# Performance work log

Hardware: AMD Instinct MI355X
Metric: run time of the kernel (lower is better)

## Reference

```python
import jax, jax.numpy as jnp
import numpy as np
from jax import lax

DIM = 128
HEADS = 4
B, H, W = 8, 128, 128


def conv1x1(x, w, b):
    # x: [B,C,H,W], w: [O,I,1,1]
    y = lax.conv_general_dilated(x, w, (1, 1), 'VALID',
                                 dimension_numbers=('NCHW', 'OIHW', 'NCHW'))
    return y + b[None, :, None, None]


def dwconv3x3(x, w, b):
    # depthwise: w: [C,1,3,3], groups=C
    C = x.shape[1]
    y = lax.conv_general_dilated(x, w, (1, 1), ((1, 1), (1, 1)),
                                 dimension_numbers=('NCHW', 'OIHW', 'NCHW'),
                                 feature_group_count=C)
    return y + b[None, :, None, None]


def setup_inputs() -> dict:
    key = jax.random.key(0)
    ks = jax.random.split(key, 7)
    s = 0.02
    return {
        'x': jax.random.normal(ks[0], (B, DIM, H, W), jnp.float32),
        'qkv_w': jax.random.normal(ks[1], (3 * DIM, DIM, 1, 1), jnp.float32) * s,
        'qkv_b': jnp.zeros((3 * DIM,), jnp.float32),
        'dw_w': jax.random.normal(ks[2], (3 * DIM, 1, 3, 3), jnp.float32) * s,
        'dw_b': jnp.zeros((3 * DIM,), jnp.float32),
        'proj_w': jax.random.normal(ks[3], (DIM, DIM, 1, 1), jnp.float32) * s,
        'proj_b': jnp.zeros((DIM,), jnp.float32),
        'temperature': jnp.ones((HEADS, 1, 1, 1), jnp.float32),
    }


def reference(x, qkv_w, qkv_b, dw_w, dw_b, proj_w, proj_b, temperature):
    b, C, h, w = x.shape
    heads = temperature.shape[0]
    c = C // heads

    qkv = dwconv3x3(conv1x1(x, qkv_w, qkv_b), dw_w, dw_b)
    q, k, v = jnp.split(qkv, 3, axis=1)

    # b (head c) h w -> b head c h w
    q = q.reshape(b, heads, c, h, w)
    k = k.reshape(b, heads, c, h, w)
    v = v.reshape(b, heads, c, h, w)

    # L2-normalize along H (axis=-2), matching torch F.normalize eps=1e-12
    eps = 1e-12
    q = q / jnp.maximum(jnp.linalg.norm(q, axis=-2, keepdims=True), eps)
    k = k / jnp.maximum(jnp.linalg.norm(k, axis=-2, keepdims=True), eps)

    # attn[b,n,c,j,k] = sum_i q[b,n,c,i,j] * k_[b,n,c,i,k]  -> [b,head,c,W,W]
    attn = jnp.einsum('bncij,bncik->bncjk', q, k) * temperature
    attn = jax.nn.softmax(attn, axis=-2)

    # out[b,n,c,i,k] = sum_j v[b,n,c,i,j] * attn[b,n,c,j,k]
    out = jnp.einsum('bncij,bncjk->bncik', v, attn)
    out = out.reshape(b, C, h, w)
    return conv1x1(out, proj_w, proj_b)
```

## Files before the change

### kernel.cpp

```cpp
#include <hip/hip_runtime.h>

typedef unsigned short u16;
typedef unsigned int   u32;

typedef short bf16x8 __attribute__((ext_vector_type(8)));
typedef float f32x4  __attribute__((ext_vector_type(4)));

__device__ __forceinline__ float bf2f(u16 u) { return __uint_as_float(((u32)u) << 16); }
__device__ __forceinline__ u16 f2bf(float f) {
    u32 u = __float_as_uint(f);
    return (u16)((u + 0x7fffu + ((u >> 16) & 1u)) >> 16);
}

#define MFMA16(a, b, c) __builtin_amdgcn_mfma_f32_16x16x32_bf16(a, b, c, 0, 0, 0)

__global__ __launch_bounds__(256, 4) void k_xpose(const float* __restrict__ x,
                                                  u16* __restrict__ xT) {
    __shared__ u16 Xs[128 * 128];
    const int ptile = blockIdx.x, b = blockIdx.y;
    const int t = threadIdx.x;
    const float* xb = x + (((size_t)b) << 21) + ptile * 128;
#pragma unroll
    for (int i = 0; i < 16; ++i) {
        int idx = i * 256 + t;
        int ci = idx >> 5, pq = idx & 31;
        float4 v = *(const float4*)(xb + (((size_t)ci) << 14) + pq * 4);
        u32 lo = (u32)f2bf(v.x) | ((u32)f2bf(v.y) << 16);
        u32 hi = (u32)f2bf(v.z) | ((u32)f2bf(v.w) << 16);
        uint2 pk; pk.x = lo; pk.y = hi;
        int cq = ci >> 3;
        *(uint2*)(&Xs[ci * 128 + ((pq ^ cq) << 2)]) = pk;
    }
    __syncthreads();
    u16* ob = xT + (((size_t)b) << 21) + ((size_t)(ptile * 128)) * 128;
#pragma unroll
    for (int j = 0; j < 8; ++j) {
        int p = j * 16 + (t >> 4), cq = t & 15;
        u16 tmp[8];
#pragma unroll
        for (int c = 0; c < 8; ++c) {
            int ci = cq * 8 + c;
            tmp[c] = Xs[ci * 128 + (((p >> 2) ^ cq) << 2) + (p & 3)];
        }
        *(uint4*)(&ob[(size_t)p * 128 + cq * 8]) = *(const uint4*)tmp;
    }
}

template <bool CM>
__global__ __launch_bounds__(512, 6) void k_qkv_t(const u16* __restrict__ xT,
                                                  const float* __restrict__ w,
                                                  const float* __restrict__ bias,
                                                  u16* __restrict__ out1,
                                                  int cgbase) {
    extern __shared__ char smem[];
    u16* Bt = (u16*)smem;
    u16* Cs = Bt + 2048 * 8;
    const int h = blockIdx.x, cg = blockIdx.y + cgbase, b = blockIdx.z;
    const int t = threadIdx.x;

    const u16* xb = xT + (((size_t)b) << 21) + (CM ? (h << 7) : (h << 14));
#pragma unroll
    for (int i = 0; i < 4; ++i) {
        int slot = i * 512 + t;
        int p = slot >> 4, g = slot & 15;
        int gg = g ^ (p & 15);
        uint4 v = *(const uint4*)(&xb[(CM ? (p << 14) : (p << 7)) + gg * 8]);
        *(uint4*)(&Bt[slot * 8]) = v;
    }

    const int wave = t >> 6, lane = t & 63, m16 = lane & 15, quad = lane >> 4;
    bf16x8 afr[4];
    {
        const float* wp0 = w + (size_t)(cg * 128 + wave * 16 + m16) * 128 + quad * 8;
#pragma unroll
        for (int kk = 0; kk < 4; ++kk) {
            float4 w0 = *(const float4*)(wp0 + kk * 32);
            float4 w1 = *(const float4*)(wp0 + kk * 32 + 4);
            bf16x8 a;
            a[0] = (short)f2bf(w0.x); a[1] = (short)f2bf(w0.y);
            a[2] = (short)f2bf(w0.z); a[3] = (short)f2bf(w0.w);
            a[4] = (short)f2bf(w1.x); a[5] = (short)f2bf(w1.y);
            a[6] = (short)f2bf(w1.z); a[7] = (short)f2bf(w1.w);
            afr[kk] = a;
        }
    }
    __syncthreads();

    f32x4 acc[8] = {};
#pragma unroll
    for (int kk = 0; kk < 4; ++kk) {
        const int g = kk * 4 + quad;
#pragma unroll
        for (int nt = 0; nt < 8; ++nt) {
            int p = nt * 16 + m16;
            bf16x8 bf = *(const bf16x8*)(&Bt[p * 128 + ((g ^ (p & 15)) << 3)]);
            acc[nt] = MFMA16(afr[kk], bf, acc[nt]);
        }
    }

    float bv[4];
#pragma unroll
    for (int r = 0; r < 4; ++r) bv[r] = bias[cg * 128 + wave * 16 + quad * 4 + r];

    u16* ob = out1 + (((size_t)(b * 384 + cg * 128)) << 14) + (h << 7);

    if (wave < 4) {
#pragma unroll
        for (int nt = 0; nt < 8; ++nt) {
            int p = nt * 16 + m16;
#pragma unroll
            for (int r = 0; r < 4; ++r)
                Cs[(wave * 16 + quad * 4 + r) * 136 + p] = f2bf(acc[nt][r] + bv[r]);
        }
    }
    __syncthreads();
#pragma unroll
    for (int it = 0; it < 2; ++it) {
        int idx = it * 512 + t;
        int co = idx >> 4, cp = idx & 15;
        *(uint4*)(&ob[((size_t)co << 14) + cp * 8]) = *(const uint4*)(&Cs[co * 136 + cp * 8]);
    }
    __syncthreads();

    if (wave >= 4) {
#pragma unroll
        for (int nt = 0; nt < 8; ++nt) {
            int p = nt * 16 + m16;
#pragma unroll
            for (int r = 0; r < 4; ++r)
                Cs[((wave - 4) * 16 + quad * 4 + r) * 136 + p] = f2bf(acc[nt][r] + bv[r]);
        }
    }
    __syncthreads();
    u16* ob2 = ob + ((size_t)64 << 14);
#pragma unroll
    for (int it = 0; it < 2; ++it) {
        int idx = it * 512 + t;
        int co = idx >> 4, cp = idx & 15;
        *(uint4*)(&ob2[((size_t)co << 14) + cp * 8]) = *(const uint4*)(&Cs[co * 136 + cp * 8]);
    }
}

__global__ __launch_bounds__(512, 4) void k_attn(const u16* __restrict__ qkv,
                                                 const float* __restrict__ dww,
                                                 const float* __restrict__ dwb,
                                                 const float* __restrict__ temp,
                                                 u16* __restrict__ outp) {
    extern __shared__ char smem[];
    u16* R0 = (u16*)smem;
    u16* Qt = (u16*)(smem + 36864);
    float* rqk = (float*)(smem + 69632);
    u16* Pt = Qt;
    u16* Osh = R0;

    const int ch = blockIdx.x, b = blockIdx.y;
    const int head = ch >> 5;
    const int t = threadIdx.x;
    const size_t qoff = ((size_t)(b * 384 + ch)) << 14;
    const size_t koff = qoff + ((size_t)128 << 14);
    const size_t voff = qoff + ((size_t)256 << 14);

    const int wave = t >> 6, lane = t & 63, m16 = lane & 15, quad = lane >> 4;
    const int wr = wave * 16 + m16;

#pragma unroll
    for (int i = 0; i < 4; ++i) {
        int idx = i * 512 + t;
        int r = idx >> 4, c16 = idx & 15;
        *(uint4*)(&R0[r * 144 + 8 + c16 * 8]) =
            *(const uint4*)(&qkv[voff + ((size_t)r << 7) + c16 * 8]);
    }
    if (t < 256) {
        int r = t >> 1, side = t & 1;
        uint4 z = {0, 0, 0, 0};
        *(uint4*)(&R0[r * 144 + side * 136]) = z;
    }
    __syncthreads();

    bf16x8 vfr[4];
    {
        float w9[9];
        const float* wp = dww + (size_t)(256 + ch) * 9;
#pragma unroll
        for (int i = 0; i < 9; ++i) w9[i] = wp[i];
        const float gb = dwb[256 + ch];
#pragma unroll
        for (int kk = 0; kk < 4; ++kk) {
            const int c0 = quad * 8 + kk * 32;
            float acc[8];
#pragma unroll
            for (int c = 0; c < 8; ++c) acc[c] = gb;
#pragma unroll
            for (int dy = 0; dy < 3; ++dy) {
                int rr = wr + dy - 1;
                if ((unsigned)rr < 128u) {
                    const u16* row = &R0[rr * 144 + 8 + c0];
                    float v0 = bf2f(row[-1]);
                    uint4 m = *(const uint4*)row;
                    float v1 = bf2f((u16)(m.x & 0xffff)), v2 = bf2f((u16)(m.x >> 16));
                    float v3 = bf2f((u16)(m.y & 0xffff)), v4 = bf2f((u16)(m.y >> 16));
                    float v5 = bf2f((u16)(m.z & 0xffff)), v6 = bf2f((u16)(m.z >> 16));
                    float v7 = bf2f((u16)(m.w & 0xffff)), v8 = bf2f((u16)(m.w >> 16));
                    float v9 = bf2f(row[8]);
                    const float w0 = w9[dy * 3], w1 = w9[dy * 3 + 1], w2 = w9[dy * 3 + 2];
                    acc[0] += w0 * v0 + w1 * v1 + w2 * v2;
                    acc[1] += w0 * v1 + w1 * v2 + w2 * v3;
                    acc[2] += w0 * v2 + w1 * v3 + w2 * v4;
                    acc[3] += w0 * v3 + w1 * v4 + w2 * v5;
                    acc[4] += w0 * v4 + w1 * v5 + w2 * v6;
                    acc[5] += w0 * v5 + w1 * v6 + w2 * v7;
                    acc[6] += w0 * v6 + w1 * v7 + w2 * v8;
                    acc[7] += w0 * v7 + w1 * v8 + w2 * v9;
                }
            }
            bf16x8 a;
#pragma unroll
            for (int c = 0; c < 8; ++c) a[c] = (short)f2bf(acc[c]);
            vfr[kk] = a;
        }
    }
    __syncthreads();

#pragma unroll
    for (int i = 0; i < 4; ++i) {
        int idx = i * 512 + t;
        int r = idx >> 4, c16 = idx & 15;
        *(uint4*)(&R0[r * 144 + 8 + c16 * 8]) =
            *(const uint4*)(&qkv[koff + ((size_t)r << 7) + c16 * 8]);
    }
    __syncthreads();

    bf16x8 kfr[4];
    float rkinv;
    {
        float w9[9];
        const float* wp = dww + (size_t)(128 + ch) * 9;
#pragma unroll
        for (int i = 0; i < 9; ++i) w9[i] = wp[i];
        const float gb = dwb[128 + ch];
        float ssq = 0.f;
#pragma unroll
        for (int kk = 0; kk < 4; ++kk) {
            const int c0 = quad * 8 + kk * 32;
            float acc[8];
#pragma unroll
            for (int c = 0; c < 8; ++c) acc[c] = gb;
#pragma unroll
            for (int pr = 0; pr < 3; ++pr) {
                int rr = wr + pr - 1;
                if ((unsigned)rr < 128u) {
                    const u16* row = &R0[rr * 144 + 8 + c0];
                    float v0 = bf2f(row[-1]);
                    uint4 m = *(const uint4*)row;
                    float v1 = bf2f((u16)(m.x & 0xffff)), v2 = bf2f((u16)(m.x >> 16));
                    float v3 = bf2f((u16)(m.y & 0xffff)), v4 = bf2f((u16)(m.y >> 16));
                    float v5 = bf2f((u16)(m.z & 0xffff)), v6 = bf2f((u16)(m.z >> 16));
                    float v7 = bf2f((u16)(m.w & 0xffff)), v8 = bf2f((u16)(m.w >> 16));
                    float v9 = bf2f(row[8]);
                    const float w0 = w9[pr], w1 = w9[3 + pr], w2 = w9[6 + pr];
                    acc[0] += w0 * v0 + w1 * v1 + w2 * v2;
                    acc[1] += w0 * v1 + w1 * v2 + w2 * v3;
                    acc[2] += w0 * v2 + w1 * v3 + w2 * v4;
                    acc[3] += w0 * v3 + w1 * v4 + w2 * v5;
                    acc[4] += w0 * v4 + w1 * v5 + w2 * v6;
                    acc[5] += w0 * v5 + w1 * v6 + w2 * v7;
                    acc[6] += w0 * v6 + w1 * v7 + w2 * v8;
                    acc[7] += w0 * v7 + w1 * v8 + w2 * v9;
                }
            }
            bf16x8 a;
#pragma unroll
            for (int c = 0; c < 8; ++c) {
                u16 uv = f2bf(acc[c]);
                a[c] = (short)uv;
                float f = bf2f(uv);
                ssq += f * f;
            }
            kfr[kk] = a;
        }
        ssq += __shfl_xor(ssq, 16);
        ssq += __shfl_xor(ssq, 32);
        rkinv = 1.0f / fmaxf(sqrtf(ssq), 1e-12f);
    }
    __syncthreads();

#pragma unroll
    for (int i = 0; i < 4; ++i) {
        int idx = i * 512 + t;
        int r = idx >> 4, c16 = idx & 15;
        *(uint4*)(&R0[r * 144 + 8 + c16 * 8]) =
            *(const uint4*)(&qkv[qoff + ((size_t)r << 7) + c16 * 8]);
    }
    __syncthreads();

    const int jr0 = t >> 4, seg = t & 15;
    {
        float w9[9];
        const float* wp = dww + (size_t)ch * 9;
#pragma unroll
        for (int i = 0; i < 9; ++i) w9[i] = wp[i];
        const float gb = dwb[ch];
#pragma unroll
        for (int pass = 0; pass < 4; ++pass) {
            const int j = pass * 32 + jr0;
            float acc[8];
#pragma unroll
            for (int c = 0; c < 8; ++c) acc[c] = gb;
#pragma unroll
            for (int pr = 0; pr < 3; ++pr) {
                int rr = j + pr - 1;
                if ((unsigned)rr < 128u) {
                    const u16* row = &R0[rr * 144 + 8 + seg * 8];
                    float v0 = bf2f(row[-1]);
                    uint4 m = *(const uint4*)row;
                    float v1 = bf2f((u16)(m.x & 0xffff)), v2 = bf2f((u16)(m.x >> 16));
                    float v3 = bf2f((u16)(m.y & 0xffff)), v4 = bf2f((u16)(m.y >> 16));
                    float v5 = bf2f((u16)(m.z & 0xffff)), v6 = bf2f((u16)(m.z >> 16));
                    float v7 = bf2f((u16)(m.w & 0xffff)), v8 = bf2f((u16)(m.w >> 16));
                    float v9 = bf2f(row[8]);
                    const float w0 = w9[pr], w1 = w9[3 + pr], w2 = w9[6 + pr];
                    acc[0] += w0 * v0 + w1 * v1 + w2 * v2;
                    acc[1] += w0 * v1 + w1 * v2 + w2 * v3;
                    acc[2] += w0 * v2 + w1 * v3 + w2 * v4;
                    acc[3] += w0 * v3 + w1 * v4 + w2 * v5;
                    acc[4] += w0 * v4 + w1 * v5 + w2 * v6;
                    acc[5] += w0 * v5 + w1 * v6 + w2 * v7;
                    acc[6] += w0 * v6 + w1 * v7 + w2 * v8;
                    acc[7] += w0 * v7 + w1 * v8 + w2 * v9;
                }
            }
            u16 tmp[8];
            float ssq = 0.f;
#pragma unroll
            for (int c = 0; c < 8; ++c) {
                u16 uv = f2bf(acc[c]);
                tmp[c] = uv;
                float f = bf2f(uv);
                ssq += f * f;
            }
            ssq += __shfl_xor(ssq, 1);
            ssq += __shfl_xor(ssq, 2);
            ssq += __shfl_xor(ssq, 4);
            ssq += __shfl_xor(ssq, 8);
            if (seg == 0) rqk[j] = ssq;
            *(uint4*)(&Qt[j * 128 + ((seg ^ (j & 15)) << 3)]) = *(const uint4*)tmp;
        }
    }
    __syncthreads();

    if (t < 128) rqk[t] = 1.0f / fmaxf(sqrtf(rqk[t]), 1e-12f);
    __syncthreads();

    f32x4 S[8] = {};
#pragma unroll
    for (int kk = 0; kk < 4; ++kk) {
        const int sw = ((kk * 4 + quad) ^ m16) << 3;
#pragma unroll
        for (int jt = 0; jt < 8; ++jt) {
            bf16x8 af = *(const bf16x8*)(&Qt[(jt * 16 + m16) * 128 + sw]);
            S[jt] = MFMA16(af, kfr[kk], S[jt]);
        }
    }

    const float sc = temp[head] * rkinv;
    float vmax = -1e30f;
#pragma unroll
    for (int jt = 0; jt < 8; ++jt)
#pragma unroll
        for (int r = 0; r < 4; ++r) {
            float v = S[jt][r] * (rqk[jt * 16 + quad * 4 + r] * sc);
            S[jt][r] = v;
            vmax = fmaxf(vmax, v);
        }
    vmax = fmaxf(vmax, __shfl_xor(vmax, 16));
    vmax = fmaxf(vmax, __shfl_xor(vmax, 32));
    float sum = 0.f;
#pragma unroll
    for (int jt = 0; jt < 8; ++jt)
#pragma unroll
        for (int r = 0; r < 4; ++r) {
            float e = __expf(S[jt][r] - vmax);
            S[jt][r] = e;
            sum += e;
        }
    sum += __shfl_xor(sum, 16);
    sum += __shfl_xor(sum, 32);
    const float inv = 1.0f / sum;

    __syncthreads();

    {
        const int k = wr;
        u16* prow = Pt + k * 128;
#pragma unroll
        for (int jt = 0; jt < 8; ++jt)
#pragma unroll
            for (int pr = 0; pr < 2; ++pr) {
                int j0w = jt * 16 + quad * 4 + pr * 2;
                u32 pk = (u32)f2bf(S[jt][pr * 2] * inv) |
                         ((u32)f2bf(S[jt][pr * 2 + 1] * inv) << 16);
                *(u32*)(prow + (((j0w >> 3) ^ (k & 15)) << 3) + (j0w & 7)) = pk;
            }
    }
    __syncthreads();

    f32x4 O[8] = {};
#pragma unroll
    for (int kk = 0; kk < 4; ++kk) {
        const int sw = ((kk * 4 + quad) ^ m16) << 3;
#pragma unroll
        for (int nt = 0; nt < 8; ++nt) {
            bf16x8 bf = *(const bf16x8*)(&Pt[(nt * 16 + m16) * 128 + sw]);
            O[nt] = MFMA16(vfr[kk], bf, O[nt]);
        }
    }
    __syncthreads();

#pragma unroll
    for (int nt = 0; nt < 8; ++nt) {
        int k = nt * 16 + m16;
#pragma unroll
        for (int r = 0; r < 4; ++r) {
            int i = wave * 16 + quad * 4 + r;
            Osh[i * 128 + (((k >> 3) ^ (i & 15)) << 3) + (k & 7)] = f2bf(O[nt][r]);
        }
    }
    __syncthreads();

    u16* ob = outp + (((size_t)(b * 128 + ch)) << 14);
#pragma unroll
    for (int it = 0; it < 4; ++it) {
        int idx = it * 512 + t;
        int row = idx >> 4, gk = idx & 15;
        uint4 v = *(const uint4*)(&Osh[row * 128 + ((gk ^ (row & 15)) << 3)]);
        *(uint4*)(&ob[(row << 7) + gk * 8]) = v;
    }
}

__global__ __launch_bounds__(512, 6) void k_proj(const u16* __restrict__ ain,
                                                 const float* __restrict__ w,
                                                 const float* __restrict__ bias,
                                                 float* __restrict__ outp) {
    extern __shared__ char smem[];
    u16* Bt = (u16*)smem;
    u16* Sg = Bt + 16384;
    const int h = blockIdx.x, b = blockIdx.y;
    const int t = threadIdx.x;

    const int ldr = t >> 4, ldj8 = t & 15;
    const int gig = t >> 7, gp = t & 127;
    const u16* gcol = &Sg[(gig * 8) * 144 + gp];
    u16* gdst = Bt + gp * 128;
#pragma unroll
    for (int ph = 0; ph < 4; ++ph) {
        int ch = ph * 32 + ldr;
        *(uint4*)(&Sg[ldr * 144 + ldj8 * 8]) =
            *(const uint4*)(&ain[(((size_t)(b * 128 + ch)) << 14) + (h << 7) + ldj8 * 8]);
        __syncthreads();
        u16 tmp[8];
#pragma unroll
        for (int c = 0; c < 8; ++c) tmp[c] = gcol[c * 144];
        int g = ph * 4 + gig;
        *(uint4*)(gdst + ((g ^ (gp & 15)) << 3)) = *(const uint4*)tmp;
        __syncthreads();
    }

    const int wave = t >> 6, lane = t & 63, m16 = lane & 15, quad = lane >> 4;
    bf16x8 afr[4];
    {
        const float* wp0 = w + (size_t)(wave * 16 + m16) * 128 + quad * 8;
#pragma unroll
        for (int kk = 0; kk < 4; ++kk) {
            float4 w0 = *(const float4*)(wp0 + kk * 32);
            float4 w1 = *(const float4*)(wp0 + kk * 32 + 4);
            bf16x8 a;
            a[0] = (short)f2bf(w0.x); a[1] = (short)f2bf(w0.y);
            a[2] = (short)f2bf(w0.z); a[3] = (short)f2bf(w0.w);
            a[4] = (short)f2bf(w1.x); a[5] = (short)f2bf(w1.y);
            a[6] = (short)f2bf(w1.z); a[7] = (short)f2bf(w1.w);
            afr[kk] = a;
        }
    }

    f32x4 acc[8] = {};
#pragma unroll
    for (int kk = 0; kk < 4; ++kk) {
        const int g = kk * 4 + quad;
#pragma unroll
        for (int nt = 0; nt < 8; ++nt) {
            int p = nt * 16 + m16;
            bf16x8 bf = *(const bf16x8*)(&Bt[p * 128 + ((g ^ (p & 15)) << 3)]);
            acc[nt] = MFMA16(afr[kk], bf, acc[nt]);
        }
    }

    float bv[4];
#pragma unroll
    for (int r = 0; r < 4; ++r) bv[r] = bias[wave * 16 + quad * 4 + r];
    float* ob = outp + (((size_t)(b * 128)) << 14) + (h << 7);
#pragma unroll
    for (int nt = 0; nt < 8; ++nt) {
        int p = nt * 16 + m16;
#pragma unroll
        for (int r = 0; r < 4; ++r) {
            int co = wave * 16 + quad * 4 + r;
            ob[((size_t)co << 14) + p] = acc[nt][r] + bv[r];
        }
    }
}

extern "C" void kernel_launch(void* const* d_in, const int* in_sizes, int n_in,
                              void* d_out, int out_size, void* d_ws, size_t ws_size,
                              hipStream_t stream) {
    const float* x      = (const float*)d_in[0];
    const float* qkv_w  = (const float*)d_in[1];
    const float* qkv_b  = (const float*)d_in[2];
    const float* dw_w   = (const float*)d_in[3];
    const float* dw_b   = (const float*)d_in[4];
    const float* proj_w = (const float*)d_in[5];
    const float* proj_b = (const float*)d_in[6];
    const float* temp   = (const float*)d_in[7];
    float* out = (float*)d_out;

    u16* buf1 = (u16*)d_ws;
    u16* buf2 = buf1 + (size_t)8 * 384 * 16384;

    hipFuncSetAttribute((const void*)k_qkv_t<true>,  hipFuncAttributeMaxDynamicSharedMemorySize, 50176);
    hipFuncSetAttribute((const void*)k_qkv_t<false>, hipFuncAttributeMaxDynamicSharedMemorySize, 50176);
    hipFuncSetAttribute((const void*)k_attn, hipFuncAttributeMaxDynamicSharedMemorySize, 70144);
    hipFuncSetAttribute((const void*)k_proj, hipFuncAttributeMaxDynamicSharedMemorySize, 41984);

    k_xpose<<<dim3(128, 8), 256, 0, stream>>>(x, buf2);
    k_qkv_t<true><<<dim3(128, 2, 8), 512, 50176, stream>>>(buf2, qkv_w, qkv_b, buf1, 0);
    k_qkv_t<false><<<dim3(128, 1, 8), 512, 50176, stream>>>(buf2, qkv_w, qkv_b, buf1, 2);
    k_attn<<<dim3(128, 8), 512, 70144, stream>>>(buf1, dw_w, dw_b, temp, buf2);
    k_proj<<<dim3(128, 8), 512, 41984, stream>>>(buf2, proj_w, proj_b, out);
}
```

Baseline: 251.7 us.

## Prefetch next K/Q tile into registers during dwconv and pad LDS row stride

In the attention kernel, the global loads for the K tile are now issued into registers before the V depthwise conv runs, and the Q tile loads are issued before the K conv. The registers are written to shared memory after the barrier, so global latency overlaps with compute. The shared-memory row stride also grows from 144 to 152 elements to reduce bank conflicts, which shifts later buffers and raises dynamic LDS by 2KB. The trade-off is more register pressure, which could hurt occupancy.

```diff
diff --git a/kernel.cpp b/kernel.cpp
--- a/kernel.cpp
+++ b/kernel.cpp
@@ -148,8 +148,8 @@
                                                  u16* __restrict__ outp) {
     extern __shared__ char smem[];
     u16* R0 = (u16*)smem;
-    u16* Qt = (u16*)(smem + 36864);
-    float* rqk = (float*)(smem + 69632);
+    u16* Qt = (u16*)(smem + 38912);
+    float* rqk = (float*)(smem + 71680);
     u16* Pt = Qt;
     u16* Osh = R0;
 
@@ -163,19 +163,25 @@
     const int wave = t >> 6, lane = t & 63, m16 = lane & 15, quad = lane >> 4;
     const int wr = wave * 16 + m16;
 
+    const int sr = t >> 4, sc16 = t & 15;
+
 #pragma unroll
     for (int i = 0; i < 4; ++i) {
-        int idx = i * 512 + t;
-        int r = idx >> 4, c16 = idx & 15;
-        *(uint4*)(&R0[r * 144 + 8 + c16 * 8]) =
-            *(const uint4*)(&qkv[voff + ((size_t)r << 7) + c16 * 8]);
+        int r = i * 32 + sr;
+        *(uint4*)(&R0[r * 152 + 8 + sc16 * 8]) =
+            *(const uint4*)(&qkv[voff + ((size_t)r << 7) + sc16 * 8]);
     }
     if (t < 256) {
         int r = t >> 1, side = t & 1;
         uint4 z = {0, 0, 0, 0};
-        *(uint4*)(&R0[r * 144 + side * 136]) = z;
-    }
-    __syncthreads();
+        *(uint4*)(&R0[r * 152 + side * 136]) = z;
+    }
+    __syncthreads();
+
+    uint4 pf[4];
+#pragma unroll
+    for (int i = 0; i < 4; ++i)
+        pf[i] = *(const uint4*)(&qkv[koff + ((size_t)(i * 32 + sr) << 7) + sc16 * 8]);
 
     bf16x8 vfr[4];
     {
@@ -194,7 +200,7 @@
             for (int dy = 0; dy < 3; ++dy) {
                 int rr = wr + dy - 1;
                 if ((unsigned)rr < 128u) {
-                    const u16* row = &R0[rr * 144 + 8 + c0];
+                    const u16* row = &R0[rr * 152 + 8 + c0];
                     float v0 = bf2f(row[-1]);
                     uint4 m = *(const uint4*)row;
                     float v1 = bf2f((u16)(m.x & 0xffff)), v2 = bf2f((u16)(m.x >> 16));
@@ -222,13 +228,13 @@
     __syncthreads();
 
 #pragma unroll
-    for (int i = 0; i < 4; ++i) {
-        int idx = i * 512 + t;
-        int r = idx >> 4, c16 = idx & 15;
-        *(uint4*)(&R0[r * 144 + 8 + c16 * 8]) =
-            *(const uint4*)(&qkv[koff + ((size_t)r << 7) + c16 * 8]);
-    }
-    __syncthreads();
+    for (int i = 0; i < 4; ++i)
+        *(uint4*)(&R0[(i * 32 + sr) * 152 + 8 + sc16 * 8]) = pf[i];
+    __syncthreads();
+
+#pragma unroll
+    for (int i = 0; i < 4; ++i)
+        pf[i] = *(const uint4*)(&qkv[qoff + ((size_t)(i * 32 + sr) << 7) + sc16 * 8]);
 
     bf16x8 kfr[4];
     float rkinv;
@@ -249,7 +255,7 @@
             for (int pr = 0; pr < 3; ++pr) {
                 int rr = wr + pr - 1;
                 if ((unsigned)rr < 128u) {
-                    const u16* row = &R0[rr * 144 + 8 + c0];
+                    const u16* row = &R0[rr * 152 + 8 + c0];
                     float v0 = bf2f(row[-1]);
                     uint4 m = *(const uint4*)row;
                     float v1 = bf2f((u16)(m.x & 0xffff)), v2 = bf2f((u16)(m.x >> 16));
@@ -285,12 +291,8 @@
     __syncthreads();
 
 #pragma unroll
-    for (int i = 0; i < 4; ++i) {
-        int idx = i * 512 + t;
-        int r = idx >> 4, c16 = idx & 15;
-        *(uint4*)(&R0[r * 144 + 8 + c16 * 8]) =
-            *(const uint4*)(&qkv[qoff + ((size_t)r << 7) + c16 * 8]);
-    }
+    for (int i = 0; i < 4; ++i)
+        *(uint4*)(&R0[(i * 32 + sr) * 152 + 8 + sc16 * 8]) = pf[i];
     __syncthreads();
 
     const int jr0 = t >> 4, seg = t & 15;
@@ -310,7 +312,7 @@
             for (int pr = 0; pr < 3; ++pr) {
                 int rr = j + pr - 1;
                 if ((unsigned)rr < 128u) {
-                    const u16* row = &R0[rr * 144 + 8 + seg * 8];
+                    const u16* row = &R0[rr * 152 + 8 + seg * 8];
                     float v0 = bf2f(row[-1]);
                     uint4 m = *(const uint4*)row;
                     float v1 = bf2f((u16)(m.x & 0xffff)), v2 = bf2f((u16)(m.x >> 16));
@@ -527,12 +529,12 @@
 
     hipFuncSetAttribute((const void*)k_qkv_t<true>,  hipFuncAttributeMaxDynamicSharedMemorySize, 50176);
     hipFuncSetAttribute((const void*)k_qkv_t<false>, hipFuncAttributeMaxDynamicSharedMemorySize, 50176);
-    hipFuncSetAttribute((const void*)k_attn, hipFuncAttributeMaxDynamicSharedMemorySize, 70144);
+    hipFuncSetAttribute((const void*)k_attn, hipFuncAttributeMaxDynamicSharedMemorySize, 72192);
     hipFuncSetAttribute((const void*)k_proj, hipFuncAttributeMaxDynamicSharedMemorySize, 41984);
 
     k_xpose<<<dim3(128, 8), 256, 0, stream>>>(x, buf2);
     k_qkv_t<true><<<dim3(128, 2, 8), 512, 50176, stream>>>(buf2, qkv_w, qkv_b, buf1, 0);
     k_qkv_t<false><<<dim3(128, 1, 8), 512, 50176, stream>>>(buf2, qkv_w, qkv_b, buf1, 2);
-    k_attn<<<dim3(128, 8), 512, 70144, stream>>>(buf1, dw_w, dw_b, temp, buf2);
+    k_attn<<<dim3(128, 8), 512, 72192, stream>>>(buf1, dw_w, dw_b, temp, buf2);
     k_proj<<<dim3(128, 8), 512, 41984, stream>>>(buf2, proj_w, proj_b, out);
 }
```

Result: slower. 261.0 us (+3.7%).
